# Kernel optimization log

Measured on AMD Instinct MI355X. Metric: run time of the kernel, lower is better.

## Reference

```python
import jax, jax.numpy as jnp
import numpy as np
import math

B, S, D = 4, 128, 2560
H, HD = 32, 80
FFN = 10240
DEC, ENC = 256, 256
EPS = 1e-5


def setup_inputs() -> dict:
    key = jax.random.key(0)
    ks = iter(jax.random.split(key, 40))

    def w(shape, scale=0.02):
        return jax.random.normal(next(ks), shape, jnp.float32) * scale

    inp = {}
    inp["x"] = jax.random.normal(next(ks), (B, S, D), jnp.float32)
    inp["xa"] = jax.random.normal(next(ks), (B, S, D), jnp.float32)
    # self-attn mask: causal over the S prefill positions, False on unfilled cache tail
    j = jnp.arange(DEC)
    i = jnp.arange(S)
    m = (j[None, :] <= i[:, None]) & (j[None, :] < S)  # [S, DEC]
    inp["mask"] = jnp.broadcast_to(m[None, None], (B, 1, S, DEC))
    inp["cross_mask"] = jnp.broadcast_to((jnp.arange(ENC) < S)[None, None, None], (B, 1, 1, ENC))
    # LayerNorms
    for n in ["ln1", "ln2", "ln3"]:
        inp[n + "_g"] = jnp.ones((D,), jnp.float32)
        inp[n + "_b"] = jnp.zeros((D,), jnp.float32)
    # self-attn projections ([in, out] layout for x @ W)
    for p in ["sa", "ca"]:
        for n in ["wq", "wk", "wv", "wo"]:
            inp[p + "_" + n] = w((D, D))
        for n in ["bq", "bk", "bv", "bo"]:
            inp[p + "_" + n] = jnp.zeros((D,), jnp.float32)
    inp["cache_sk"] = jnp.zeros((B, H, DEC, HD), jnp.float32)
    inp["cache_sv"] = jnp.zeros((B, H, DEC, HD), jnp.float32)
    inp["cache_ck"] = jnp.zeros((B, H, ENC, HD), jnp.float32)
    inp["cache_cv"] = jnp.zeros((B, H, ENC, HD), jnp.float32)
    inp["fc1_w"] = w((D, FFN))
    inp["fc1_b"] = jnp.zeros((FFN,), jnp.float32)
    inp["fc2_w"] = w((FFN, D))
    inp["fc2_b"] = jnp.zeros((D,), jnp.float32)
    return inp


def _ln(h, g, b):
    h32 = h.astype(jnp.float32)
    mu = h32.mean(-1, keepdims=True)
    var = ((h32 - mu) ** 2).mean(-1, keepdims=True)
    return ((h32 - mu) * jax.lax.rsqrt(var + EPS) * g + b).astype(h.dtype)


def _heads(t):
    b, s, _ = t.shape
    return t.reshape(b, s, H, HD).transpose(0, 2, 1, 3)  # [B,H,S,HD]


def _attn(q, k_cache, v_cache, mask):
    kf = k_cache.astype(q.dtype)
    vf = v_cache.astype(q.dtype)
    scores = jnp.einsum("bhqd,bhkd->bhqk", q, kf) / math.sqrt(HD)
    if mask is not None:
        scores = jnp.where(mask, scores, jnp.finfo(scores.dtype).min)
    attn = jax.nn.softmax(scores.astype(jnp.float32), axis=-1).astype(q.dtype)
    o = jnp.einsum("bhqk,bhkd->bhqd", attn, vf)
    b, h, s, hd = o.shape
    return o.transpose(0, 2, 1, 3).reshape(b, s, h * hd)


def reference(x, xa, mask, cross_mask,
              ln1_g, ln1_b, sa_wq, sa_bq, sa_wk, sa_bk, sa_wv, sa_bv, sa_wo, sa_bo,
              cache_sk, cache_sv,
              ln2_g, ln2_b, ca_wq, ca_bq, ca_wk, ca_bk, ca_wv, ca_bv, ca_wo, ca_bo,
              cache_ck, cache_cv,
              ln3_g, ln3_b, fc1_w, fc1_b, fc2_w, fc2_b):
    # --- self-attention (prefill path: scatter with arange indices = prefix write) ---
    h = _ln(x, ln1_g, ln1_b)
    q = _heads(h @ sa_wq + sa_bq)
    k = _heads(h @ sa_wk + sa_bk)
    v = _heads(h @ sa_wv + sa_bv)
    s = q.shape[2]
    sk = cache_sk.at[:, :, :s, :].set(k.astype(jnp.float32))
    sv = cache_sv.at[:, :, :s, :].set(v.astype(jnp.float32))
    o = _attn(q, sk, sv, mask)
    x = x + (o @ sa_wo + sa_bo)

    # --- cross-attention: K/V from encoder output, scattered into cache ---
    h = _ln(x, ln2_g, ln2_b)
    q = _heads(h @ ca_wq + ca_bq)
    k = _heads(xa @ ca_wk + ca_bk)
    v = _heads(xa @ ca_wv + ca_bv)
    kv = k.shape[2]
    ck = cache_ck.at[:, :, :kv, :].set(k.astype(jnp.float32))
    cv = cache_cv.at[:, :, :kv, :].set(v.astype(jnp.float32))
    o = _attn(q, ck, cv, cross_mask)
    x = x + (o @ ca_wo + ca_bo)

    # --- MLP: fc1 -> GELU (exact) -> fc2 ---
    h = _ln(x, ln3_g, ln3_b)
    x = x + (jax.nn.gelu(h @ fc1_w + fc1_b, approximate=False) @ fc2_w + fc2_b)
    return (x, sk, sv, ck, cv)
```

## Files before the change

### kernel.cpp

```cpp
#include <hip/hip_runtime.h>
#include <hip/hip_bf16.h>
#include <math.h>

#define TB   4
#define TS   128
#define TD   2560
#define TH   32
#define THD  80
#define TFFN 10240
#define TDEC 256
#define TM   (TB * TS)
#define CACHE_N ((size_t)TB * TH * TDEC * THD)

using short8  = __attribute__((ext_vector_type(8))) short;
using sshort4 = __attribute__((ext_vector_type(4))) short;
using floatx4 = __attribute__((ext_vector_type(4))) float;

__device__ __forceinline__ short f2bf(float f) {
  unsigned u = __builtin_bit_cast(unsigned, f);
  u += 0x7fff + ((u >> 16) & 1);
  return (short)(u >> 16);
}
__device__ __forceinline__ float bf2f(short s) {
  unsigned u = ((unsigned)(unsigned short)s) << 16;
  return __builtin_bit_cast(float, u);
}

struct TArgs {
  const float* src[10];
  short*       dst[10];
  int ntiles[10];
  int tstart[10];
};

__global__ __launch_bounds__(256, 8)
void wtrans_kernel(TArgs t)
{
  __shared__ short tile[64][74];
  const int bid = blockIdx.x;
  int j = 0;
#pragma unroll
  for (int i = 1; i < 10; ++i) if (bid >= t.tstart[i]) j = i;
  const int rel = bid - t.tstart[j];
  const int nt  = t.ntiles[j];
  const int kt  = rel / nt, ntile = rel - kt * nt;
  const float* src = t.src[j];
  short* dst = t.dst[j];
  const int N = nt * 64;
  const int K = gridDim.x ? 0 : 0;
  (void)K;
  const int ktiles = ((j + 1 < 10 ? t.tstart[j + 1] : (int)gridDim.x) - t.tstart[j]) / nt;
  const int Kdim = ktiles * 64;
  const int k0 = kt * 64, n0 = ntile * 64;
  const int tid = threadIdx.x;
  const int rr = tid >> 4;
  const int cc = (tid & 15) * 4;
#pragma unroll
  for (int it = 0; it < 4; ++it) {
    const int k = rr + it * 16;
    float4 v = *(const float4*)(src + (size_t)(k0 + k) * N + n0 + cc);
    tile[k][cc]     = f2bf(v.x);
    tile[k][cc + 1] = f2bf(v.y);
    tile[k][cc + 2] = f2bf(v.z);
    tile[k][cc + 3] = f2bf(v.w);
  }
  __syncthreads();
#pragma unroll
  for (int it = 0; it < 4; ++it) {
    const int n = rr + it * 16;
    sshort4 o;
    o[0] = tile[cc][n]; o[1] = tile[cc + 1][n];
    o[2] = tile[cc + 2][n]; o[3] = tile[cc + 3][n];
    *(sshort4*)(dst + (size_t)(n0 + n) * Kdim + k0 + cc) = o;
  }
}

struct GArgs {
  const short* A[3];
  const short* B[3];
  float*       outf[3];
  int tilesPerSeg;
  int nx;
  int N;
  int lda;
  int Kc;
};

__device__ __forceinline__ void stage_load(const short* __restrict__ A,
                                           const short* __restrict__ B,
                                           int lda, int m0, int n0, int k0,
                                           int tid, short8 ra[2], short8 rb[2])
{
  const int cb = (tid & 3) * 8;
  const int rr = tid >> 2;
#pragma unroll
  for (int it = 0; it < 2; ++it) {
    ra[it] = *(const short8*)(A + (size_t)(m0 + rr + it * 64) * lda + k0 + cb);
    rb[it] = *(const short8*)(B + (size_t)(n0 + rr + it * 64) * lda + k0 + cb);
  }
}

__device__ __forceinline__ void stage_commit(short* __restrict__ As, short* __restrict__ Bs,
                                             int tid, const short8 ra[2], const short8 rb[2])
{
  const int cb = (tid & 3) * 8;
  const int rr = tid >> 2;
#pragma unroll
  for (int it = 0; it < 2; ++it) {
    *(short8*)(&As[(rr + it * 64) * 40 + cb]) = ra[it];
    *(short8*)(&Bs[(rr + it * 64) * 40 + cb]) = rb[it];
  }
}

__device__ __forceinline__ void compute_step(const short* __restrict__ As,
                                             const short* __restrict__ Bs,
                                             int wm, int wn, int lr, int lq,
                                             floatx4 acc[4][4])
{
  short8 af[4], bfr[4];
#pragma unroll
  for (int t = 0; t < 4; ++t)
    af[t] = *(const short8*)(&As[(wm + t * 16 + lr) * 40 + lq * 8]);
#pragma unroll
  for (int t = 0; t < 4; ++t)
    bfr[t] = *(const short8*)(&Bs[(wn + t * 16 + lr) * 40 + lq * 8]);
#pragma unroll
  for (int tm = 0; tm < 4; ++tm)
#pragma unroll
    for (int tn = 0; tn < 4; ++tn)
      acc[tm][tn] = __builtin_amdgcn_mfma_f32_16x16x32_bf16(af[tm], bfr[tn],
                                                            acc[tm][tn], 0, 0, 0);
}

__global__ __launch_bounds__(256, 3)
void gemmF(GArgs g)
{
  __shared__ short As[128 * 40];
  __shared__ short Bs[128 * 40];

  const int raw = blockIdx.x;
  const int grp = ((raw >> 5) << 3) | (raw & 7);
  const int my  = (raw >> 3) & 3;
  const int z   = grp / g.nx;
  const int x   = grp - z * g.nx;
  const int seg = x / g.tilesPerSeg;
  const int tx  = x - seg * g.tilesPerSeg;

  const short* A = g.A[seg];
  const short* B = g.B[seg];
  const int N = g.N, lda = g.lda;
  const int m0 = my * 128;
  const int n0 = tx * 128;
  const int k0base = z * g.Kc;
  const int nk = g.Kc / 32;

  const int tid = threadIdx.x;
  const int lane = tid & 63;
  const int wv = tid >> 6;
  const int wm = (wv >> 1) * 64;
  const int wn = (wv & 1) * 64;
  const int lr = lane & 15;
  const int lq = lane >> 4;

  floatx4 acc[4][4];
#pragma unroll
  for (int i = 0; i < 4; ++i)
#pragma unroll
    for (int j = 0; j < 4; ++j)
      acc[i][j] = floatx4{0.f, 0.f, 0.f, 0.f};

  short8 raP[2], raF[2], rbP[2], rbF[2];

  stage_load(A, B, lda, m0, n0, k0base, tid, raP, rbP);
  stage_commit(As, Bs, tid, raP, rbP);
  __syncthreads();
  stage_load(A, B, lda, m0, n0, k0base + 32, tid, raP, rbP);

  for (int ki = 0; ki < nk; ki += 2) {
    if (ki + 2 < nk)
      stage_load(A, B, lda, m0, n0, k0base + (ki + 2) * 32, tid, raF, rbF);
    compute_step(As, Bs, wm, wn, lr, lq, acc);
    __syncthreads();
    stage_commit(As, Bs, tid, raP, rbP);
    __syncthreads();

    if (ki + 3 < nk)
      stage_load(A, B, lda, m0, n0, k0base + (ki + 3) * 32, tid, raP, rbP);
    compute_step(As, Bs, wm, wn, lr, lq, acc);
    if (ki + 2 < nk) {
      __syncthreads();
      stage_commit(As, Bs, tid, raF, rbF);
      __syncthreads();
    }
  }

  float* outf = g.outf[seg];
#pragma unroll
  for (int tm = 0; tm < 4; ++tm) {
#pragma unroll
    for (int tn = 0; tn < 4; ++tn) {
      const int col = n0 + wn + tn * 16 + lr;
#pragma unroll
      for (int r = 0; r < 4; ++r) {
        const int row = m0 + wm + tm * 16 + lq * 4 + r;
        outf[(size_t)z * TM * N + (size_t)row * N + col] = acc[tm][tn][r];
      }
    }
  }
}

template<int Z>
__global__ void qkv_combine_kernel(const float* __restrict__ p,
                                   const float* __restrict__ bq,
                                   const float* __restrict__ bk,
                                   const float* __restrict__ bv,
                                   float* __restrict__ qbuf,
                                   float* __restrict__ sk,
                                   float* __restrict__ sv)
{
  const int i4 = blockIdx.x * 256 + threadIdx.x;
  const int row = i4 / 1920;
  const int c4  = i4 - row * 1920;
  const int col = c4 * 4;
  const int seg = (col >= 2 * TD) ? 2 : (col >= TD ? 1 : 0);
  const int c   = col - seg * TD;
  const float* base = p + (size_t)seg * ((size_t)Z * TM * TD) + (size_t)row * TD + c;
  float4 v = *(const float4*)base;
#pragma unroll
  for (int zz = 1; zz < Z; ++zz) {
    float4 t = *(const float4*)(base + (size_t)zz * TM * TD);
    v.x += t.x; v.y += t.y; v.z += t.z; v.w += t.w;
  }
  const float* bias = (seg == 0) ? bq : (seg == 1 ? bk : bv);
  float4 b4 = *(const float4*)(bias + c);
  v.x += b4.x; v.y += b4.y; v.z += b4.z; v.w += b4.w;
  if (seg == 0) {
    *(float4*)(qbuf + (size_t)row * TD + c) = v;
  } else {
    const int hh = c / THD, hd = c % THD;
    const int b = row >> 7, sI = row & 127;
    float* dst = (seg == 1) ? sk : sv;
    *(float4*)(dst + (((size_t)(b * TH + hh) * TDEC + sI) * THD + hd)) = v;
  }
}

template<int Z>
__global__ void fc1_gelu_kernel(const float* __restrict__ p,
                                const float* __restrict__ bias,
                                short* __restrict__ out)
{
  const int i4 = blockIdx.x * 256 + threadIdx.x;
  const int row = i4 / (TFFN / 4);
  const int c4  = i4 - row * (TFFN / 4);
  const int col = c4 * 4;
  const size_t idx = (size_t)row * TFFN + col;
  float4 v = *(const float4*)(p + idx);
#pragma unroll
  for (int zz = 1; zz < Z; ++zz) {
    float4 t = *(const float4*)(p + (size_t)zz * TM * TFFN + idx);
    v.x += t.x; v.y += t.y; v.z += t.z; v.w += t.w;
  }
  float4 b4 = *(const float4*)(bias + col);
  v.x += b4.x; v.y += b4.y; v.z += b4.z; v.w += b4.w;
  sshort4 o;
  o[0] = f2bf(0.5f * v.x * (1.0f + erff(v.x * 0.70710678118654752f)));
  o[1] = f2bf(0.5f * v.y * (1.0f + erff(v.y * 0.70710678118654752f)));
  o[2] = f2bf(0.5f * v.z * (1.0f + erff(v.z * 0.70710678118654752f)));
  o[3] = f2bf(0.5f * v.w * (1.0f + erff(v.w * 0.70710678118654752f)));
  *(sshort4*)(out + idx) = o;
}

template<bool CAUSAL>
__global__ __launch_bounds__(256, 2)
void attn_kernel(const float* __restrict__ q, const float* __restrict__ kc,
                 const float* __restrict__ vc, short* __restrict__ ob)
{
  __shared__ short kb[TS * THD];
  __shared__ short vb[TS * THD];
  __shared__ float qf[64 * 84];
  short* pb = (short*)qf;

  const int tid = threadIdx.x;
  const int bh = blockIdx.x;
  const int b = bh >> 5, h = bh & 31;
  const int r0 = blockIdx.y * 64;

  const size_t cbase = (size_t)bh * TDEC * THD;
  for (int idx = tid; idx < TS * THD; idx += 256) {
    kb[idx] = f2bf(kc[cbase + idx]);
    vb[idx] = f2bf(vc[cbase + idx]);
  }
  for (int idx = tid; idx < 64 * THD; idx += 256) {
    int r = idx / THD, d = idx - r * THD;
    qf[r * 84 + d] = q[(size_t)(b * TS + r0 + r) * TD + h * THD + d];
  }
  __syncthreads();

  const int r = tid >> 2;
  const int quarter = tid & 3;
  const int qi = r0 + r;

  float sc[32];
#pragma unroll 1
  for (int jj = 0; jj < 32; ++jj) {
    int j = quarter + jj * 4;
    if (CAUSAL && j > qi) { sc[jj] = -1e30f; continue; }
    float a = 0.f;
#pragma unroll 8
    for (int d = 0; d < THD; ++d)
      a += qf[r * 84 + d] * bf2f(kb[j * THD + d]);
    sc[jj] = a * 0.11180339887498949f;
  }

  float mx = -1e30f;
#pragma unroll
  for (int jj = 0; jj < 32; ++jj) mx = fmaxf(mx, sc[jj]);
  mx = fmaxf(mx, __shfl_xor(mx, 1));
  mx = fmaxf(mx, __shfl_xor(mx, 2));
  float sum = 0.f;
#pragma unroll
  for (int jj = 0; jj < 32; ++jj) { sc[jj] = __expf(sc[jj] - mx); sum += sc[jj]; }
  sum += __shfl_xor(sum, 1);
  sum += __shfl_xor(sum, 2);
  const float rinv = 1.0f / sum;

  __syncthreads();
#pragma unroll
  for (int jj = 0; jj < 32; ++jj)
    pb[r * TS + quarter + jj * 4] = f2bf(sc[jj] * rinv);
  __syncthreads();

  for (int it = 0; it < 20; ++it) {
    int idx = tid + it * 256;
    int rr = idx / THD, d = idx - rr * THD;
    float a = 0.f;
#pragma unroll 8
    for (int j = 0; j < TS; ++j)
      a += bf2f(pb[rr * TS + j]) * bf2f(vb[j * THD + d]);
    ob[(size_t)(b * TS + r0 + rr) * TD + h * THD + d] = f2bf(a);
  }
}

__global__ __launch_bounds__(256, 4)
void ln_kernel(const float* __restrict__ x, const float* __restrict__ g,
               const float* __restrict__ bb, short* __restrict__ out)
{
  const int row = blockIdx.x;
  const float* xr = x + (size_t)row * TD;
  const int tid = threadIdx.x;
  float vals[10];
  float s = 0.f, ss = 0.f;
#pragma unroll
  for (int it = 0; it < 10; ++it) {
    float v = xr[tid + it * 256];
    vals[it] = v; s += v; ss += v * v;
  }
#pragma unroll
  for (int o = 32; o > 0; o >>= 1) { s += __shfl_xor(s, o); ss += __shfl_xor(ss, o); }
  __shared__ float red[8];
  const int wv = tid >> 6, lane = tid & 63;
  if (lane == 0) { red[wv] = s; red[wv + 4] = ss; }
  __syncthreads();
  s  = red[0] + red[1] + red[2] + red[3];
  ss = red[4] + red[5] + red[6] + red[7];
  const float mu = s * (1.0f / TD);
  const float rstd = rsqrtf(ss * (1.0f / TD) - mu * mu + 1e-5f);
  short* orow = out + (size_t)row * TD;
#pragma unroll
  for (int it = 0; it < 10; ++it) {
    int i = tid + it * 256;
    orow[i] = f2bf((vals[it] - mu) * rstd * g[i] + bb[i]);
  }
}

template<int Z>
__global__ __launch_bounds__(256, 4)
void ln_fuse_kernel(const float* __restrict__ xin, const float* __restrict__ p,
                    const float* __restrict__ obias,
                    const float* __restrict__ g, const float* __restrict__ bb,
                    short* __restrict__ hout, float* __restrict__ xout)
{
  const int row = blockIdx.x;
  const int tid = threadIdx.x;
  const size_t base = (size_t)row * TD;
  float vals[10];
  float s = 0.f, ss = 0.f;
#pragma unroll
  for (int it = 0; it < 10; ++it) {
    int i = tid + it * 256;
    float v = xin[base + i] + obias[i];
#pragma unroll
    for (int zz = 0; zz < Z; ++zz)
      v += p[(size_t)zz * TM * TD + base + i];
    vals[it] = v; xout[base + i] = v; s += v; ss += v * v;
  }
#pragma unroll
  for (int o = 32; o > 0; o >>= 1) { s += __shfl_xor(s, o); ss += __shfl_xor(ss, o); }
  __shared__ float red[8];
  const int wv = tid >> 6, lane = tid & 63;
  if (lane == 0) { red[wv] = s; red[wv + 4] = ss; }
  __syncthreads();
  s  = red[0] + red[1] + red[2] + red[3];
  ss = red[4] + red[5] + red[6] + red[7];
  const float mu = s * (1.0f / TD);
  const float rstd = rsqrtf(ss * (1.0f / TD) - mu * mu + 1e-5f);
#pragma unroll
  for (int it = 0; it < 10; ++it) {
    int i = tid + it * 256;
    hout[base + i] = f2bf((vals[it] - mu) * rstd * g[i] + bb[i]);
  }
}

template<int Z>
__global__ void fc2_combine_kernel(const float* __restrict__ x2, const float* __restrict__ p,
                                   const float* __restrict__ bias, float* __restrict__ out)
{
  const size_t i = ((size_t)blockIdx.x * 256 + threadIdx.x) * 4;
  const int col = (int)(i % TD);
  float4 v = *(const float4*)(x2 + i);
#pragma unroll
  for (int zz = 0; zz < Z; ++zz) {
    float4 t = *(const float4*)(p + (size_t)zz * TM * TD + i);
    v.x += t.x; v.y += t.y; v.z += t.z; v.w += t.w;
  }
  float4 b4 = *(const float4*)(bias + col);
  v.x += b4.x; v.y += b4.y; v.z += b4.z; v.w += b4.w;
  *(float4*)(out + i) = v;
}

__global__ void cvt_bf16_kernel(const float* __restrict__ in, short* __restrict__ out, int n)
{
  int i = blockIdx.x * 256 + threadIdx.x;
  if (i < n) out[i] = f2bf(in[i]);
}

__global__ void tailcopy_kernel(const float* __restrict__ src, float* __restrict__ dst)
{
  int off4 = blockIdx.x * 256 + threadIdx.x;
  int chunk = blockIdx.y;
  size_t pos = (size_t)chunk * 5120 + 2560 + off4;
  ((float4*)dst)[pos] = ((const float4*)src)[pos];
}

extern "C" void kernel_launch(void* const* d_in, const int* in_sizes, int n_in,
                              void* d_out, int out_size, void* d_ws, size_t ws_size,
                              hipStream_t stream)
{
  (void)in_sizes; (void)n_in; (void)out_size; (void)ws_size;
  const float* x        = (const float*)d_in[0];
  const float* xa       = (const float*)d_in[1];
  const float* ln1_g    = (const float*)d_in[4];
  const float* ln1_b    = (const float*)d_in[5];
  const float* ln2_g    = (const float*)d_in[6];
  const float* ln2_b    = (const float*)d_in[7];
  const float* ln3_g    = (const float*)d_in[8];
  const float* ln3_b    = (const float*)d_in[9];
  const float* sa_wq    = (const float*)d_in[10];
  const float* sa_wk    = (const float*)d_in[11];
  const float* sa_wv    = (const float*)d_in[12];
  const float* sa_wo    = (const float*)d_in[13];
  const float* sa_bq    = (const float*)d_in[14];
  const float* sa_bk    = (const float*)d_in[15];
  const float* sa_bv    = (const float*)d_in[16];
  const float* sa_bo    = (const float*)d_in[17];
  const float* ca_wq    = (const float*)d_in[18];
  const float* ca_wk    = (const float*)d_in[19];
  const float* ca_wv    = (const float*)d_in[20];
  const float* ca_wo    = (const float*)d_in[21];
  const float* ca_bq    = (const float*)d_in[22];
  const float* ca_bk    = (const float*)d_in[23];
  const float* ca_bv    = (const float*)d_in[24];
  const float* ca_bo    = (const float*)d_in[25];
  const float* cache_sk = (const float*)d_in[26];
  const float* cache_sv = (const float*)d_in[27];
  const float* cache_ck = (const float*)d_in[28];
  const float* cache_cv = (const float*)d_in[29];
  const float* fc1_w    = (const float*)d_in[30];
  const float* fc1_b    = (const float*)d_in[31];
  const float* fc2_w    = (const float*)d_in[32];
  const float* fc2_b    = (const float*)d_in[33];

  float* out_x  = (float*)d_out;
  float* out_sk = out_x + (size_t)TM * TD;
  float* out_sv = out_sk + CACHE_N;
  float* out_ck = out_sv + CACHE_N;
  float* out_cv = out_ck + CACHE_N;

  char* w = (char*)d_ws;
  short* h_b   = (short*)w; w += (size_t)TM * TD * 2;
  short* xa_b  = (short*)w; w += (size_t)TM * TD * 2;
  short* o_b   = (short*)w; w += (size_t)TM * TD * 2;
  short* ffn_b = (short*)w; w += (size_t)TM * TFFN * 2;
  float* qbuf  = (float*)w; w += (size_t)TM * TD * 4;
  float* x1    = (float*)w; w += (size_t)TM * TD * 4;
  float* x2    = (float*)w; w += (size_t)TM * TD * 4;
  float* pbuf  = (float*)w; w += (size_t)TM * TD * 4 * 12;
  short* sa_wqT = (short*)w; w += (size_t)TD * TD * 2;
  short* sa_wkT = (short*)w; w += (size_t)TD * TD * 2;
  short* sa_wvT = (short*)w; w += (size_t)TD * TD * 2;
  short* sa_woT = (short*)w; w += (size_t)TD * TD * 2;
  short* ca_wqT = (short*)w; w += (size_t)TD * TD * 2;
  short* ca_wkT = (short*)w; w += (size_t)TD * TD * 2;
  short* ca_wvT = (short*)w; w += (size_t)TD * TD * 2;
  short* ca_woT = (short*)w; w += (size_t)TD * TD * 2;
  short* fc1_wT = (short*)w; w += (size_t)TD * TFFN * 2;
  short* fc2_wT = (short*)w; w += (size_t)TD * TFFN * 2;

  const dim3 blk(256);
  const dim3 gAttn(TB * TH, 2);

  {
    TArgs t{};
    const float* s[10] = {sa_wq, sa_wk, sa_wv, sa_wo, ca_wq, ca_wk, ca_wv, ca_wo, fc1_w, fc2_w};
    short* d[10]       = {sa_wqT, sa_wkT, sa_wvT, sa_woT, ca_wqT, ca_wkT, ca_wvT, ca_woT, fc1_wT, fc2_wT};
    int nt[10]         = {40, 40, 40, 40, 40, 40, 40, 40, 160, 40};
    int kt[10]         = {40, 40, 40, 40, 40, 40, 40, 40, 40, 160};
    int cum = 0;
    for (int i = 0; i < 10; ++i) {
      t.src[i] = s[i]; t.dst[i] = d[i]; t.ntiles[i] = nt[i];
      t.tstart[i] = cum; cum += nt[i] * kt[i];
    }
    wtrans_kernel<<<dim3(cum), blk, 0, stream>>>(t);
  }

  cvt_bf16_kernel<<<dim3(TM * TD / 256), blk, 0, stream>>>(xa, xa_b, TM * TD);
  tailcopy_kernel<<<dim3(10, TB * TH), blk, 0, stream>>>(cache_sk, out_sk);
  tailcopy_kernel<<<dim3(10, TB * TH), blk, 0, stream>>>(cache_sv, out_sv);
  tailcopy_kernel<<<dim3(10, TB * TH), blk, 0, stream>>>(cache_ck, out_ck);
  tailcopy_kernel<<<dim3(10, TB * TH), blk, 0, stream>>>(cache_cv, out_cv);

  ln_kernel<<<dim3(TM), blk, 0, stream>>>(x, ln1_g, ln1_b, h_b);
  {
    GArgs a{};
    a.A[0] = h_b; a.B[0] = sa_wqT; a.outf[0] = pbuf;
    a.A[1] = h_b; a.B[1] = sa_wkT; a.outf[1] = pbuf + (size_t)4 * TM * TD;
    a.A[2] = h_b; a.B[2] = sa_wvT; a.outf[2] = pbuf + (size_t)8 * TM * TD;
    a.tilesPerSeg = 20; a.nx = 60; a.N = TD; a.lda = TD; a.Kc = TD / 4;
    gemmF<<<dim3(960), blk, 0, stream>>>(a);
  }
  qkv_combine_kernel<4><<<dim3(TM * 7680 / 4 / 256), blk, 0, stream>>>(
      pbuf, sa_bq, sa_bk, sa_bv, qbuf, out_sk, out_sv);
  attn_kernel<true><<<gAttn, blk, 0, stream>>>(qbuf, out_sk, out_sv, o_b);
  {
    GArgs a{};
    a.A[0] = o_b; a.B[0] = sa_woT; a.outf[0] = pbuf;
    a.tilesPerSeg = 20; a.nx = 20; a.N = TD; a.lda = TD; a.Kc = TD / 8;
    gemmF<<<dim3(640), blk, 0, stream>>>(a);
  }
  ln_fuse_kernel<8><<<dim3(TM), blk, 0, stream>>>(x, pbuf, sa_bo, ln2_g, ln2_b, h_b, x1);

  {
    GArgs a{};
    a.A[0] = h_b;  a.B[0] = ca_wqT; a.outf[0] = pbuf;
    a.A[1] = xa_b; a.B[1] = ca_wkT; a.outf[1] = pbuf + (size_t)4 * TM * TD;
    a.A[2] = xa_b; a.B[2] = ca_wvT; a.outf[2] = pbuf + (size_t)8 * TM * TD;
    a.tilesPerSeg = 20; a.nx = 60; a.N = TD; a.lda = TD; a.Kc = TD / 4;
    gemmF<<<dim3(960), blk, 0, stream>>>(a);
  }
  qkv_combine_kernel<4><<<dim3(TM * 7680 / 4 / 256), blk, 0, stream>>>(
      pbuf, ca_bq, ca_bk, ca_bv, qbuf, out_ck, out_cv);
  attn_kernel<false><<<gAttn, blk, 0, stream>>>(qbuf, out_ck, out_cv, o_b);
  {
    GArgs a{};
    a.A[0] = o_b; a.B[0] = ca_woT; a.outf[0] = pbuf;
    a.tilesPerSeg = 20; a.nx = 20; a.N = TD; a.lda = TD; a.Kc = TD / 8;
    gemmF<<<dim3(640), blk, 0, stream>>>(a);
  }
  ln_fuse_kernel<8><<<dim3(TM), blk, 0, stream>>>(x1, pbuf, ca_bo, ln3_g, ln3_b, h_b, x2);

  {
    GArgs a{};
    a.A[0] = h_b; a.B[0] = fc1_wT; a.outf[0] = pbuf;
    a.tilesPerSeg = 80; a.nx = 80; a.N = TFFN; a.lda = TD; a.Kc = TD / 2;
    gemmF<<<dim3(640), blk, 0, stream>>>(a);
  }
  fc1_gelu_kernel<2><<<dim3(TM * TFFN / 4 / 256), blk, 0, stream>>>(pbuf, fc1_b, ffn_b);
  {
    GArgs a{};
    a.A[0] = ffn_b; a.B[0] = fc2_wT; a.outf[0] = pbuf;
    a.tilesPerSeg = 20; a.nx = 20; a.N = TD; a.lda = TFFN; a.Kc = TFFN / 8;
    gemmF<<<dim3(640), blk, 0, stream>>>(a);
  }
  fc2_combine_kernel<8><<<dim3(TM * TD / 4 / 256), blk, 0, stream>>>(x2, pbuf, fc2_b, out_x);
}
```

Baseline: 935.5 us.

## Use async global-to-LDS double buffering in GEMM and pack pairs in weight transpose

The bf16 GEMM's register-staged prefetch is replaced with direct global-to-LDS async loads (global_load_lds) into two LDS buffers, so only one barrier is needed per k-step. The LDS rows lose their padding, which suits the contiguous per-lane layout these loads require but may raise LDS bank conflicts on the MFMA fragment reads. The launch bound moves to 4 blocks per CU. The weight transpose kernel now handles 128x64 tiles and packs two bf16 k-values into each 32-bit word, making its LDS traffic and global stores wider.

```diff
diff --git a/kernel.cpp b/kernel.cpp
--- a/kernel.cpp
+++ b/kernel.cpp
@@ -26,52 +26,63 @@
   return __builtin_bit_cast(float, u);
 }
 
+__device__ __forceinline__ void async16(void* lds, const void* g) {
+  __builtin_amdgcn_global_load_lds(
+      (const __attribute__((address_space(1))) unsigned int*)g,
+      (__attribute__((address_space(3))) unsigned int*)lds, 16, 0, 0);
+}
+
 struct TArgs {
   const float* src[10];
-  short*       dst[10];
-  int ntiles[10];
+  unsigned*    dst[10];
+  int n64[10];
+  int k2[10];
   int tstart[10];
 };
 
 __global__ __launch_bounds__(256, 8)
 void wtrans_kernel(TArgs t)
 {
-  __shared__ short tile[64][74];
+  __shared__ unsigned t32[64 * 69];
   const int bid = blockIdx.x;
   int j = 0;
 #pragma unroll
   for (int i = 1; i < 10; ++i) if (bid >= t.tstart[i]) j = i;
   const int rel = bid - t.tstart[j];
-  const int nt  = t.ntiles[j];
-  const int kt  = rel / nt, ntile = rel - kt * nt;
+  const int nb  = t.n64[j];
+  const int bk  = rel / nb, bn = rel - bk * nb;
   const float* src = t.src[j];
-  short* dst = t.dst[j];
-  const int N = nt * 64;
-  const int K = gridDim.x ? 0 : 0;
-  (void)K;
-  const int ktiles = ((j + 1 < 10 ? t.tstart[j + 1] : (int)gridDim.x) - t.tstart[j]) / nt;
-  const int Kdim = ktiles * 64;
-  const int k0 = kt * 64, n0 = ntile * 64;
+  unsigned* dst = t.dst[j];
+  const int N  = nb * 64;
+  const int K2 = t.k2[j];
+  const int k0 = bk * 128, n0 = bn * 64;
   const int tid = threadIdx.x;
-  const int rr = tid >> 4;
-  const int cc = (tid & 15) * 4;
+
 #pragma unroll
   for (int it = 0; it < 4; ++it) {
-    const int k = rr + it * 16;
-    float4 v = *(const float4*)(src + (size_t)(k0 + k) * N + n0 + cc);
-    tile[k][cc]     = f2bf(v.x);
-    tile[k][cc + 1] = f2bf(v.y);
-    tile[k][cc + 2] = f2bf(v.z);
-    tile[k][cc + 3] = f2bf(v.w);
+    const int kk = (tid >> 4) + it * 16;
+    const int n4 = (tid & 15) * 4;
+    const float* s0 = src + (size_t)(k0 + 2 * kk) * N + n0 + n4;
+    float4 a = *(const float4*)s0;
+    float4 b = *(const float4*)(s0 + N);
+    uint4 p;
+    p.x = (unsigned)(unsigned short)f2bf(a.x) | ((unsigned)(unsigned short)f2bf(b.x) << 16);
+    p.y = (unsigned)(unsigned short)f2bf(a.y) | ((unsigned)(unsigned short)f2bf(b.y) << 16);
+    p.z = (unsigned)(unsigned short)f2bf(a.z) | ((unsigned)(unsigned short)f2bf(b.z) << 16);
+    p.w = (unsigned)(unsigned short)f2bf(a.w) | ((unsigned)(unsigned short)f2bf(b.w) << 16);
+    *(uint4*)(&t32[kk * 69 + n4]) = p;
   }
   __syncthreads();
 #pragma unroll
   for (int it = 0; it < 4; ++it) {
-    const int n = rr + it * 16;
-    sshort4 o;
-    o[0] = tile[cc][n]; o[1] = tile[cc + 1][n];
-    o[2] = tile[cc + 2][n]; o[3] = tile[cc + 3][n];
-    *(sshort4*)(dst + (size_t)(n0 + n) * Kdim + k0 + cc) = o;
+    const int n  = (tid >> 4) + it * 16;
+    const int k4 = (tid & 15) * 4;
+    uint4 o;
+    o.x = t32[(k4 + 0) * 69 + n];
+    o.y = t32[(k4 + 1) * 69 + n];
+    o.z = t32[(k4 + 2) * 69 + n];
+    o.w = t32[(k4 + 3) * 69 + n];
+    *(uint4*)(dst + (size_t)(n0 + n) * K2 + bk * 64 + k4) = o;
   }
 }
 
@@ -86,29 +97,18 @@
   int Kc;
 };
 
-__device__ __forceinline__ void stage_load(const short* __restrict__ A,
-                                           const short* __restrict__ B,
+__device__ __forceinline__ void stage_tile(const short* __restrict__ Ag,
+                                           const short* __restrict__ Bg,
                                            int lda, int m0, int n0, int k0,
-                                           int tid, short8 ra[2], short8 rb[2])
-{
-  const int cb = (tid & 3) * 8;
-  const int rr = tid >> 2;
-#pragma unroll
-  for (int it = 0; it < 2; ++it) {
-    ra[it] = *(const short8*)(A + (size_t)(m0 + rr + it * 64) * lda + k0 + cb);
-    rb[it] = *(const short8*)(B + (size_t)(n0 + rr + it * 64) * lda + k0 + cb);
-  }
-}
-
-__device__ __forceinline__ void stage_commit(short* __restrict__ As, short* __restrict__ Bs,
-                                             int tid, const short8 ra[2], const short8 rb[2])
-{
-  const int cb = (tid & 3) * 8;
-  const int rr = tid >> 2;
-#pragma unroll
-  for (int it = 0; it < 2; ++it) {
-    *(short8*)(&As[(rr + it * 64) * 40 + cb]) = ra[it];
-    *(short8*)(&Bs[(rr + it * 64) * 40 + cb]) = rb[it];
+                                           short* As, short* Bs, int w, int l)
+{
+#pragma unroll
+  for (int j = 0; j < 2; ++j) {
+    const int chunk = w * 2 + j;
+    const int r = chunk * 16 + (l >> 2);
+    const int c = (l & 3) * 8;
+    async16(As + chunk * 512, Ag + (size_t)(m0 + r) * lda + k0 + c);
+    async16(Bs + chunk * 512, Bg + (size_t)(n0 + r) * lda + k0 + c);
   }
 }
 
@@ -120,10 +120,10 @@
   short8 af[4], bfr[4];
 #pragma unroll
   for (int t = 0; t < 4; ++t)
-    af[t] = *(const short8*)(&As[(wm + t * 16 + lr) * 40 + lq * 8]);
+    af[t] = *(const short8*)(As + (wm + t * 16 + lr) * 32 + lq * 8);
 #pragma unroll
   for (int t = 0; t < 4; ++t)
-    bfr[t] = *(const short8*)(&Bs[(wn + t * 16 + lr) * 40 + lq * 8]);
+    bfr[t] = *(const short8*)(Bs + (wn + t * 16 + lr) * 32 + lq * 8);
 #pragma unroll
   for (int tm = 0; tm < 4; ++tm)
 #pragma unroll
@@ -132,11 +132,11 @@
                                                             acc[tm][tn], 0, 0, 0);
 }
 
-__global__ __launch_bounds__(256, 3)
+__global__ __launch_bounds__(256, 4)
 void gemmF(GArgs g)
 {
-  __shared__ short As[128 * 40];
-  __shared__ short Bs[128 * 40];
+  __shared__ short As[2][128 * 32];
+  __shared__ short Bs[2][128 * 32];
 
   const int raw = blockIdx.x;
   const int grp = ((raw >> 5) << 3) | (raw & 7);
@@ -169,29 +169,16 @@
     for (int j = 0; j < 4; ++j)
       acc[i][j] = floatx4{0.f, 0.f, 0.f, 0.f};
 
-  short8 raP[2], raF[2], rbP[2], rbF[2];
-
-  stage_load(A, B, lda, m0, n0, k0base, tid, raP, rbP);
-  stage_commit(As, Bs, tid, raP, rbP);
-  __syncthreads();
-  stage_load(A, B, lda, m0, n0, k0base + 32, tid, raP, rbP);
-
-  for (int ki = 0; ki < nk; ki += 2) {
-    if (ki + 2 < nk)
-      stage_load(A, B, lda, m0, n0, k0base + (ki + 2) * 32, tid, raF, rbF);
-    compute_step(As, Bs, wm, wn, lr, lq, acc);
+  stage_tile(A, B, lda, m0, n0, k0base, As[0], Bs[0], wv, lane);
+  __syncthreads();
+
+  for (int ki = 0; ki < nk; ++ki) {
+    const int cur = ki & 1;
+    if (ki + 1 < nk)
+      stage_tile(A, B, lda, m0, n0, k0base + (ki + 1) * 32,
+                 As[cur ^ 1], Bs[cur ^ 1], wv, lane);
+    compute_step(As[cur], Bs[cur], wm, wn, lr, lq, acc);
     __syncthreads();
-    stage_commit(As, Bs, tid, raP, rbP);
-    __syncthreads();
-
-    if (ki + 3 < nk)
-      stage_load(A, B, lda, m0, n0, k0base + (ki + 3) * 32, tid, raP, rbP);
-    compute_step(As, Bs, wm, wn, lr, lq, acc);
-    if (ki + 2 < nk) {
-      __syncthreads();
-      stage_commit(As, Bs, tid, raF, rbF);
-      __syncthreads();
-    }
   }
 
   float* outf = g.outf[seg];
@@ -503,7 +490,7 @@
   short* ca_wkT = (short*)w; w += (size_t)TD * TD * 2;
   short* ca_wvT = (short*)w; w += (size_t)TD * TD * 2;
   short* ca_woT = (short*)w; w += (size_t)TD * TD * 2;
-  short* fc1_wT = (short*)w; w += (size_t)TD * TFFN * 2;
+  short* fc1_wT = (short*)w; w += (size_t)TFFN * TD * 2;
   short* fc2_wT = (short*)w; w += (size_t)TD * TFFN * 2;
 
   const dim3 blk(256);
@@ -513,12 +500,13 @@
     TArgs t{};
     const float* s[10] = {sa_wq, sa_wk, sa_wv, sa_wo, ca_wq, ca_wk, ca_wv, ca_wo, fc1_w, fc2_w};
     short* d[10]       = {sa_wqT, sa_wkT, sa_wvT, sa_woT, ca_wqT, ca_wkT, ca_wvT, ca_woT, fc1_wT, fc2_wT};
-    int nt[10]         = {40, 40, 40, 40, 40, 40, 40, 40, 160, 40};
-    int kt[10]         = {40, 40, 40, 40, 40, 40, 40, 40, 40, 160};
+    int N_[10] = {TD, TD, TD, TD, TD, TD, TD, TD, TFFN, TD};
+    int K_[10] = {TD, TD, TD, TD, TD, TD, TD, TD, TD, TFFN};
     int cum = 0;
     for (int i = 0; i < 10; ++i) {
-      t.src[i] = s[i]; t.dst[i] = d[i]; t.ntiles[i] = nt[i];
-      t.tstart[i] = cum; cum += nt[i] * kt[i];
+      t.src[i] = s[i]; t.dst[i] = (unsigned*)d[i];
+      t.n64[i] = N_[i] / 64; t.k2[i] = K_[i] / 2;
+      t.tstart[i] = cum; cum += (K_[i] / 128) * (N_[i] / 64);
     }
     wtrans_kernel<<<dim3(cum), blk, 0, stream>>>(t);
   }
```

After: 949.9 us. Within noise of the previous version (+1.5%).
